# Kernel optimization log

Measured on AMD Instinct MI355X. Metric: run time of the kernel, lower is better.

The kernel has to match this reference:

```python
import jax, jax.numpy as jnp
import numpy as np

N = 100000
NNZ = 3200000
K = 3

def setup_inputs() -> dict:
    key = jax.random.key(0)
    ks = jax.random.split(key, 9)
    return {
        "x": jax.random.normal(ks[0], (N, 128), dtype=jnp.float32),
        "vals": jax.random.uniform(ks[1], (NNZ,), dtype=jnp.float32) * (1.0 / 32.0),
        "W1": jax.random.normal(ks[2], (128 * K, 256), dtype=jnp.float32) * 0.05,
        "b1": jax.random.normal(ks[3], (256,), dtype=jnp.float32) * 0.05,
        "W2": jax.random.normal(ks[4], (256 * K, 64), dtype=jnp.float32) * 0.05,
        "b2": jax.random.normal(ks[5], (64,), dtype=jnp.float32) * 0.05,
        "rows": jax.random.randint(ks[6], (NNZ,), 0, N, dtype=jnp.int32),
        "cols": jax.random.randint(ks[7], (NNZ,), 0, N, dtype=jnp.int32),
        "idx": jax.random.randint(ks[8], (50000,), 0, N, dtype=jnp.int32),
    }

def _spmm(rows, cols, vals, x):
    # sparse [N,N] @ dense [N,F] via gather + segment_sum
    return jax.ops.segment_sum(vals[:, None] * x[cols], rows, num_segments=N)

def _cheb_basis(x, rows, cols, vals, k):
    # Chebyshev recurrence: T0=x, T1=L x, T_m = 2 L T_{m-1} - T_{m-2}
    xs = [x]
    if k > 1:
        x0, x1 = x, _spmm(rows, cols, vals, x)
        xs.append(x1)
        for _ in range(2, k):
            x2 = 2.0 * _spmm(rows, cols, vals, x1) - x0
            xs.append(x2)
            x0, x1 = x1, x2
    # match torch layout: [N, F, K] -> [N, F*K] (per-feature K contiguous)
    return jnp.stack(xs, axis=2).reshape(x.shape[0], -1)

def reference(x, vals, W1, b1, W2, b2, rows, cols, idx):
    h = _cheb_basis(x, rows, cols, vals, K) @ W1 + b1
    h = jax.nn.relu(h)  # dropout omitted (eval mode)
    out = _cheb_basis(h, rows, cols, vals, K) @ W2 + b2
    return out[idx]
```

## Files before the change

kernel.cpp:

```cpp
#include <hip/hip_runtime.h>
#include <hip/hip_bf16.h>

typedef __attribute__((ext_vector_type(8))) __bf16 bf16x8;
typedef __attribute__((ext_vector_type(4))) float floatx4;
typedef unsigned short ushort_t;
typedef unsigned int uint_t;

#define N_NODES 100000
#define NNZ_E   3200000
#define N_IDX   50000
#define NB_BKT  196
#define PTILE   8192
#define PBLOCKS 391

__device__ __forceinline__ float bf2f(uint_t u16) {
  union { float f; uint_t i; } v; v.i = u16 << 16; return v.f;
}
__device__ __forceinline__ unsigned short f2bf(float f) {
  union { float f; uint_t i; } v; v.f = f;
  uint_t x = v.i;
  return (unsigned short)((x + 0x7FFFu + ((x >> 16) & 1u)) >> 16);
}
__device__ __forceinline__ uint_t pk(float lo, float hi) {
  return ((uint_t)f2bf(hi) << 16) | (uint_t)f2bf(lo);
}


__global__ __launch_bounds__(256) void k_bhist(const int* __restrict__ rows,
                                               int* __restrict__ bcnt) {
  __shared__ int h[NB_BKT];
  for (int i = threadIdx.x; i < NB_BKT; i += 256) h[i] = 0;
  __syncthreads();
  int base = blockIdx.x * PTILE;
  for (int i = threadIdx.x; i < PTILE; i += 256) {
    int e = base + i;
    if (e < NNZ_E) atomicAdd(&h[rows[e] >> 9], 1);
  }
  __syncthreads();
  for (int i = threadIdx.x; i < NB_BKT; i += 256)
    if (h[i]) atomicAdd(&bcnt[i], h[i]);
}

__global__ void k_bscan(const int* __restrict__ bcnt, int* __restrict__ bbase,
                        int* __restrict__ bcur) {
  __shared__ int ts[256];
  int t = threadIdx.x;
  int v = (t < NB_BKT) ? bcnt[t] : 0;
  ts[t] = v;
  __syncthreads();
  for (int off = 1; off < 256; off <<= 1) {
    int x = ts[t];
    int a = (t >= off) ? ts[t - off] : 0;
    __syncthreads();
    ts[t] = x + a;
    __syncthreads();
  }
  if (t < NB_BKT) {
    int b = (t == 0) ? 0 : ts[t - 1];
    bbase[t] = b;
    bcur[t] = b;
  }
}

__global__ __launch_bounds__(256) void k_part(const int* __restrict__ rows,
                                              const int* __restrict__ cols,
                                              const float* __restrict__ vals,
                                              int* __restrict__ bcur,
                                              int2* __restrict__ tmp) {
  __shared__ int h[NB_BKT];
  for (int i = threadIdx.x; i < NB_BKT; i += 256) h[i] = 0;
  __syncthreads();
  int base = blockIdx.x * PTILE;
  for (int i = threadIdx.x; i < PTILE; i += 256) {
    int e = base + i;
    if (e < NNZ_E) atomicAdd(&h[rows[e] >> 9], 1);
  }
  __syncthreads();
  for (int i = threadIdx.x; i < NB_BKT; i += 256) {
    int c = h[i];
    h[i] = c ? atomicAdd(&bcur[i], c) : 0;
  }
  __syncthreads();
  for (int i = threadIdx.x; i < PTILE; i += 256) {
    int e = base + i;
    if (e < NNZ_E) {
      int rr = rows[e];
      int p = atomicAdd(&h[rr >> 9], 1);
      int2 o;
      o.x = cols[e] | ((rr & 511) << 17);
      o.y = __float_as_int(vals[e]);
      tmp[p] = o;
    }
  }
}

__global__ __launch_bounds__(512) void k_sort(const int* __restrict__ bbase,
                                              const int2* __restrict__ tmp,
                                              int2* __restrict__ edges,
                                              int* __restrict__ rowptr) {
  __shared__ int cnt[512];
  __shared__ int ts[512];
  int b = blockIdx.x, t = threadIdx.x;
  int s = bbase[b];
  int epos = (b == NB_BKT - 1) ? NNZ_E : bbase[b + 1];
  cnt[t] = 0;
  __syncthreads();
  for (int i = s + t; i < epos; i += 512)
    atomicAdd(&cnt[(tmp[i].x >> 17) & 511], 1);
  __syncthreads();
  ts[t] = cnt[t];
  __syncthreads();
  for (int off = 1; off < 512; off <<= 1) {
    int x = ts[t];
    int a = (t >= off) ? ts[t - off] : 0;
    __syncthreads();
    ts[t] = x + a;
    __syncthreads();
  }
  int pre = (t == 0) ? 0 : ts[t - 1];
  int grow = b * 512 + t;
  if (grow < N_NODES) rowptr[grow] = s + pre;
  cnt[t] = s + pre;
  __syncthreads();
  for (int i = s + t; i < epos; i += 512) {
    int2 p = tmp[i];
    int rl = (p.x >> 17) & 511;
    int pos = atomicAdd(&cnt[rl], 1);
    int2 o;
    o.x = p.x & 0x1FFFF;
    o.y = p.y;
    edges[pos] = o;
  }
  if (b == 0 && t == 0) rowptr[N_NODES] = NNZ_E;
}


__global__ __launch_bounds__(256) void k_prep(
    const float4* __restrict__ x, const float* __restrict__ W1,
    const float* __restrict__ W2, ushort4* __restrict__ xb,
    ushort_t* __restrict__ W1p, ushort_t* __restrict__ W2p) {
  int b = blockIdx.x;
  if (b < 12500) {
    int i = b * 256 + threadIdx.x;
    float4 v = x[i];
    ushort4 o;
    o.x = f2bf(v.x); o.y = f2bf(v.y); o.z = f2bf(v.z); o.w = f2bf(v.w);
    xb[i] = o;
  } else if (b < 12884) {
    int kp = b - 12500;
    int n  = threadIdx.x;
    int ch = kp >> 7;
    int f  = kp & 127;
    float v;
    if (ch == 0)      v = W1[(f*3+0)*256+n] - W1[(f*3+2)*256+n];
    else if (ch == 1) v = W1[(f*3+1)*256+n];
    else              v = 2.0f * W1[(f*3+2)*256+n];
    int kb = kp >> 5, kr = kp & 31;
    int lane = ((kr >> 3) << 4) | (n & 15);
    W1p[(((size_t)kb * 16 + (n >> 4)) * 64 + lane) * 8 + (kr & 7)] = f2bf(v);
  } else {
    int f = b - 12884;
    int c = threadIdx.x;
    if (c < 192) {
      int g = c >> 6, n = c & 63;
      float v;
      if (g == 0)      v = W2[(f*3+0)*64+n] - W2[(f*3+2)*64+n];
      else if (g == 1) v = W2[(f*3+1)*64+n];
      else             v = 2.0f * W2[(f*3+2)*64+n];
      int kb = f >> 5, kr = f & 31;
      int nb = c >> 4;
      int lane = ((kr >> 3) << 4) | (c & 15);
      W2p[(((size_t)kb * 12 + nb) * 64 + lane) * 8 + (kr & 7)] = f2bf(v);
    }
  }
}


__global__ __launch_bounds__(256) void k_spmm128(
    const int* __restrict__ rowptr, const int2* __restrict__ edges,
    const ushort_t* __restrict__ in, ushort_t* __restrict__ out) {
  int r = __builtin_amdgcn_readfirstlane(blockIdx.x * 4 + (threadIdx.x >> 6));
  int f = threadIdx.x & 63;
  int e0 = rowptr[r], e1 = rowptr[r + 1];
  float a0 = 0.f, a1 = 0.f;
  int e = e0;
  for (; e + 16 <= e1; e += 16) {
    int2 E[16];
#pragma unroll
    for (int j = 0; j < 16; ++j) E[j] = edges[e + j];
    uint_t q[16];
#pragma unroll
    for (int j = 0; j < 16; ++j)
      q[j] = *(const uint_t*)(in + (size_t)E[j].x * 128 + 2 * f);
#pragma unroll
    for (int j = 0; j < 16; ++j) {
      float v = __int_as_float(E[j].y);
      a0 = fmaf(v, bf2f(q[j] & 0xFFFFu), a0);
      a1 = fmaf(v, bf2f(q[j] >> 16), a1);
    }
  }
  for (; e + 4 <= e1; e += 4) {
    int2 E[4];
#pragma unroll
    for (int j = 0; j < 4; ++j) E[j] = edges[e + j];
    uint_t q[4];
#pragma unroll
    for (int j = 0; j < 4; ++j)
      q[j] = *(const uint_t*)(in + (size_t)E[j].x * 128 + 2 * f);
#pragma unroll
    for (int j = 0; j < 4; ++j) {
      float v = __int_as_float(E[j].y);
      a0 = fmaf(v, bf2f(q[j] & 0xFFFFu), a0);
      a1 = fmaf(v, bf2f(q[j] >> 16), a1);
    }
  }
  for (; e < e1; ++e) {
    int2 E = edges[e];
    uint_t q = *(const uint_t*)(in + (size_t)E.x * 128 + 2 * f);
    float v = __int_as_float(E.y);
    a0 = fmaf(v, bf2f(q & 0xFFFFu), a0);
    a1 = fmaf(v, bf2f(q >> 16), a1);
  }
  uint_t o = ((uint_t)f2bf(a1) << 16) | (uint_t)f2bf(a0);
  *(uint_t*)(out + (size_t)r * 128 + 2 * f) = o;
}


__global__ __launch_bounds__(256) void k_spmm64_add(
    const int* __restrict__ rowptr, const int2* __restrict__ edges,
    const ushort_t* __restrict__ p2, const ushort_t* __restrict__ p1,
    ushort_t* __restrict__ u) {
  int r = __builtin_amdgcn_readfirstlane(blockIdx.x * 4 + (threadIdx.x >> 6));
  int lane = threadIdx.x & 63;
  int half = lane >> 5, l5 = lane & 31;
  int e0 = rowptr[r], e1 = rowptr[r + 1];
  float a0 = 0.f, a1 = 0.f;
  int e = e0;
  for (; e + 16 <= e1; e += 16) {
    int2 Ea[8], Eb[8];
#pragma unroll
    for (int j = 0; j < 8; ++j) { Ea[j] = edges[e + 2*j]; Eb[j] = edges[e + 2*j + 1]; }
    uint_t q[8];
#pragma unroll
    for (int j = 0; j < 8; ++j) {
      int c = half ? Eb[j].x : Ea[j].x;
      q[j] = *(const uint_t*)(p2 + (size_t)c * 64 + 2 * l5);
    }
#pragma unroll
    for (int j = 0; j < 8; ++j) {
      float v = __int_as_float(half ? Eb[j].y : Ea[j].y);
      a0 = fmaf(v, bf2f(q[j] & 0xFFFFu), a0);
      a1 = fmaf(v, bf2f(q[j] >> 16), a1);
    }
  }
  for (; e + 2 <= e1; e += 2) {
    int2 Ea = edges[e], Eb = edges[e + 1];
    int c = half ? Eb.x : Ea.x;
    uint_t q = *(const uint_t*)(p2 + (size_t)c * 64 + 2 * l5);
    float v = __int_as_float(half ? Eb.y : Ea.y);
    a0 = fmaf(v, bf2f(q & 0xFFFFu), a0);
    a1 = fmaf(v, bf2f(q >> 16), a1);
  }
  if (e < e1) {
    int2 Ea = edges[e];
    uint_t q = *(const uint_t*)(p2 + (size_t)Ea.x * 64 + 2 * l5);
    float v = half ? 0.f : __int_as_float(Ea.y);
    a0 = fmaf(v, bf2f(q & 0xFFFFu), a0);
    a1 = fmaf(v, bf2f(q >> 16), a1);
  }
  a0 += __shfl_xor(a0, 32);
  a1 += __shfl_xor(a1, 32);
  if (half == 0) {
    uint_t pp = *(const uint_t*)(p1 + (size_t)r * 64 + 2 * l5);
    float b0 = a0 + bf2f(pp & 0xFFFFu);
    float b1 = a1 + bf2f(pp >> 16);
    *(uint_t*)(u + (size_t)r * 64 + 2 * l5) = pk(b0, b1);
  }
}


__global__ __launch_bounds__(256) void k_spmm64_idx(
    const int* __restrict__ rowptr, const int2* __restrict__ edges,
    const ushort_t* __restrict__ u, const float* __restrict__ p0,
    const int* __restrict__ idx, float* __restrict__ out) {
  int o = __builtin_amdgcn_readfirstlane(blockIdx.x * 4 + (threadIdx.x >> 6));
  int lane = threadIdx.x & 63;
  int half = lane >> 5, l5 = lane & 31;
  int r = __builtin_amdgcn_readfirstlane(idx[o]);
  int e0 = rowptr[r], e1 = rowptr[r + 1];
  float a0 = 0.f, a1 = 0.f;
  int e = e0;
  for (; e + 16 <= e1; e += 16) {
    int2 Ea[8], Eb[8];
#pragma unroll
    for (int j = 0; j < 8; ++j) { Ea[j] = edges[e + 2*j]; Eb[j] = edges[e + 2*j + 1]; }
    uint_t q[8];
#pragma unroll
    for (int j = 0; j < 8; ++j) {
      int c = half ? Eb[j].x : Ea[j].x;
      q[j] = *(const uint_t*)(u + (size_t)c * 64 + 2 * l5);
    }
#pragma unroll
    for (int j = 0; j < 8; ++j) {
      float v = __int_as_float(half ? Eb[j].y : Ea[j].y);
      a0 = fmaf(v, bf2f(q[j] & 0xFFFFu), a0);
      a1 = fmaf(v, bf2f(q[j] >> 16), a1);
    }
  }
  for (; e + 2 <= e1; e += 2) {
    int2 Ea = edges[e], Eb = edges[e + 1];
    int c = half ? Eb.x : Ea.x;
    uint_t q = *(const uint_t*)(u + (size_t)c * 64 + 2 * l5);
    float v = __int_as_float(half ? Eb.y : Ea.y);
    a0 = fmaf(v, bf2f(q & 0xFFFFu), a0);
    a1 = fmaf(v, bf2f(q >> 16), a1);
  }
  if (e < e1) {
    int2 Ea = edges[e];
    uint_t q = *(const uint_t*)(u + (size_t)Ea.x * 64 + 2 * l5);
    float v = half ? 0.f : __int_as_float(Ea.y);
    a0 = fmaf(v, bf2f(q & 0xFFFFu), a0);
    a1 = fmaf(v, bf2f(q >> 16), a1);
  }
  a0 += __shfl_xor(a0, 32);
  a1 += __shfl_xor(a1, 32);
  if (half == 0) {
    float2 b = *(const float2*)(p0 + (size_t)r * 64 + 2 * l5);
    float2 ww; ww.x = b.x + a0; ww.y = b.y + a1;
    *(float2*)(out + (size_t)o * 64 + 2 * l5) = ww;
  }
}


__global__ __launch_bounds__(256) void k_gemm1(
    const ushort_t* __restrict__ A0, const ushort_t* __restrict__ A1,
    const ushort_t* __restrict__ A2, const ushort_t* __restrict__ Bp,
    const float* __restrict__ bias, ushort_t* __restrict__ h) {
  int lane = threadIdx.x & 63;
  int ng = threadIdx.x >> 6;
  int r0 = blockIdx.x * 64;
  int mrl = lane & 15;
  int ko = (lane >> 4) << 3;
  floatx4 acc[4][4] = {};
#pragma unroll
  for (int kbg = 0; kbg < 12; ++kbg) {
    int c = kbg >> 2, kb = kbg & 3;
    const ushort_t* Asrc = (c == 0 ? A0 : c == 1 ? A1 : A2);
    bf16x8 a[4];
#pragma unroll
    for (int mi = 0; mi < 4; ++mi) {
      int mr = r0 + mi * 16 + mrl;
      if (mr > N_NODES - 1) mr = N_NODES - 1;
      a[mi] = *(const bf16x8*)(Asrc + (size_t)mr * 128 + kb * 32 + ko);
    }
    const ushort_t* Bb = Bp + (((size_t)(kbg * 16 + ng * 4)) * 64 + lane) * 8;
#pragma unroll
    for (int nt = 0; nt < 4; ++nt) {
      bf16x8 b = *(const bf16x8*)(Bb + (size_t)nt * 64 * 8);
#pragma unroll
      for (int mi = 0; mi < 4; ++mi)
        acc[mi][nt] = __builtin_amdgcn_mfma_f32_16x16x32_bf16(a[mi], b, acc[mi][nt], 0, 0, 0);
    }
  }
  int col0 = ng * 64 + (lane & 15);
  int rr0 = (lane >> 4) << 2;
#pragma unroll
  for (int nt = 0; nt < 4; ++nt) {
    int col = col0 + nt * 16;
    float bv = bias[col];
#pragma unroll
    for (int mi = 0; mi < 4; ++mi) {
      int rb = r0 + mi * 16 + rr0;
#pragma unroll
      for (int rg = 0; rg < 4; ++rg) {
        int row = rb + rg;
        if (row < N_NODES) {
          float v = acc[mi][nt][rg] + bv;
          v = v > 0.f ? v : 0.f;
          h[(size_t)row * 256 + col] = f2bf(v);
        }
      }
    }
  }
}


__global__ __launch_bounds__(256) void k_gemm2(
    const ushort_t* __restrict__ A, const ushort_t* __restrict__ Bp,
    const float* __restrict__ bias, float* __restrict__ p0,
    ushort_t* __restrict__ p1, ushort_t* __restrict__ p2) {
  int wid = (blockIdx.x * 256 + threadIdx.x) >> 6;
  int lane = threadIdx.x & 63;
  int mt4 = wid / 3, ng = wid - mt4 * 3;
  if (mt4 >= 1563) return;
  int r0 = mt4 * 64;
  int mrl = lane & 15;
  int ko = (lane >> 4) << 3;
  floatx4 acc[4][4] = {};
#pragma unroll
  for (int kb = 0; kb < 8; ++kb) {
    bf16x8 a[4];
#pragma unroll
    for (int mi = 0; mi < 4; ++mi) {
      int mr = r0 + mi * 16 + mrl;
      if (mr > N_NODES - 1) mr = N_NODES - 1;
      a[mi] = *(const bf16x8*)(A + (size_t)mr * 256 + kb * 32 + ko);
    }
    const ushort_t* Bb = Bp + (((size_t)(kb * 12 + ng * 4)) * 64 + lane) * 8;
#pragma unroll
    for (int nt = 0; nt < 4; ++nt) {
      bf16x8 b = *(const bf16x8*)(Bb + (size_t)nt * 64 * 8);
#pragma unroll
      for (int mi = 0; mi < 4; ++mi)
        acc[mi][nt] = __builtin_amdgcn_mfma_f32_16x16x32_bf16(a[mi], b, acc[mi][nt], 0, 0, 0);
    }
  }
  int c16 = lane & 15;
  int rr0 = (lane >> 4) << 2;
  if (ng == 0) {
#pragma unroll
    for (int nt = 0; nt < 4; ++nt) {
      float bv = bias[nt * 16 + c16];
#pragma unroll
      for (int mi = 0; mi < 4; ++mi) {
        int rb = r0 + mi * 16 + rr0;
#pragma unroll
        for (int rg = 0; rg < 4; ++rg) {
          int row = rb + rg;
          if (row < N_NODES)
            p0[(size_t)row * 64 + nt * 16 + c16] = acc[mi][nt][rg] + bv;
        }
      }
    }
  } else {
    ushort_t* dst = (ng == 1) ? p1 : p2;
#pragma unroll
    for (int nt = 0; nt < 4; ++nt)
#pragma unroll
      for (int mi = 0; mi < 4; ++mi) {
        int rb = r0 + mi * 16 + rr0;
#pragma unroll
        for (int rg = 0; rg < 4; ++rg) {
          int row = rb + rg;
          if (row < N_NODES)
            dst[(size_t)row * 64 + nt * 16 + c16] = f2bf(acc[mi][nt][rg]);
        }
      }
  }
}


extern "C" void kernel_launch(void* const* d_in, const int* in_sizes, int n_in,
                              void* d_out, int out_size, void* d_ws, size_t ws_size,
                              hipStream_t stream) {
  const float* x    = (const float*)d_in[0];
  const float* vals = (const float*)d_in[1];
  const float* W1   = (const float*)d_in[2];
  const float* b1   = (const float*)d_in[3];
  const float* W2   = (const float*)d_in[4];
  const float* b2   = (const float*)d_in[5];
  const int*   rows = (const int*)d_in[6];
  const int*   cols = (const int*)d_in[7];
  const int*   idx  = (const int*)d_in[8];
  float* out = (float*)d_out;

  char* w = (char*)d_ws;
  size_t off = 0;
  auto take = [&](size_t b) -> char* {
    char* p = w + off;
    off += (b + 255) & ~(size_t)255;
    return p;
  };
  int*      bcnt    = (int*)take((size_t)NB_BKT * 4);
  int*      bbase   = (int*)take((size_t)NB_BKT * 4);
  int*      bcur    = (int*)take((size_t)NB_BKT * 4);
  int*      rowptr  = (int*)take((size_t)(N_NODES + 1) * 4);
  int2*     tmp     = (int2*)take((size_t)NNZ_E * 8);
  int2*     edges   = (int2*)take((size_t)NNZ_E * 8);
  ushort_t* xb      = (ushort_t*)take((size_t)N_NODES * 128 * 2);
  ushort_t* T1a     = (ushort_t*)take((size_t)N_NODES * 128 * 2);
  ushort_t* U1      = (ushort_t*)take((size_t)N_NODES * 128 * 2);
  ushort_t* h       = (ushort_t*)take((size_t)N_NODES * 256 * 2);
  ushort_t* W1p     = (ushort_t*)take((size_t)384 * 256 * 2);
  ushort_t* W2p     = (ushort_t*)take((size_t)256 * 192 * 2);

  float*    p0 = (float*)xb;
  ushort_t* p1 = T1a;
  ushort_t* p2 = T1a + (size_t)N_NODES * 64;
  ushort_t* u  = U1;

  hipMemsetAsync(bcnt, 0, (size_t)NB_BKT * 4, stream);
  k_bhist<<<PBLOCKS, 256, 0, stream>>>(rows, bcnt);
  k_bscan<<<1, 256, 0, stream>>>(bcnt, bbase, bcur);
  k_part<<<PBLOCKS, 256, 0, stream>>>(rows, cols, vals, bcur, tmp);
  k_sort<<<NB_BKT, 512, 0, stream>>>(bbase, tmp, edges, rowptr);

  k_prep<<<13140, 256, 0, stream>>>((const float4*)x, W1, W2, (ushort4*)xb, W1p, W2p);

  k_spmm128<<<N_NODES / 4, 256, 0, stream>>>(rowptr, edges, xb, T1a);
  k_spmm128<<<N_NODES / 4, 256, 0, stream>>>(rowptr, edges, T1a, U1);
  k_gemm1<<<1563, 256, 0, stream>>>(xb, T1a, U1, W1p, b1, h);

  k_gemm2<<<1173, 256, 0, stream>>>(h, W2p, b2, p0, p1, p2);
  k_spmm64_add<<<N_NODES / 4, 256, 0, stream>>>(rowptr, edges, p2, p1, u);
  k_spmm64_idx<<<N_IDX / 4, 256, 0, stream>>>(rowptr, edges, u, p0, idx, out);
}
```

Measured before the change: 675.3 us.

## Split 128-wide SpMM into feature halves with dual-edge lanes per wavefront

New measurement: 680.5 us. About the same (+0.8%).

```diff
diff --git a/kernel.cpp b/kernel.cpp
--- a/kernel.cpp
+++ b/kernel.cpp
@@ -176,53 +176,56 @@
 }
 
 
-__global__ __launch_bounds__(256) void k_spmm128(
+__global__ __launch_bounds__(256) void k_spmm128h(
     const int* __restrict__ rowptr, const int2* __restrict__ edges,
     const ushort_t* __restrict__ in, ushort_t* __restrict__ out) {
-  int r = __builtin_amdgcn_readfirstlane(blockIdx.x * 4 + (threadIdx.x >> 6));
-  int f = threadIdx.x & 63;
+  int bid = blockIdx.x;
+  int hf = (bid >= 25000) ? 1 : 0;
+  int rb = bid - hf * 25000;
+  int w = threadIdx.x >> 6;
+  int r = __builtin_amdgcn_readfirstlane(rb * 4 + w);
+  int lane = threadIdx.x & 63;
+  int half = lane >> 5, l5 = lane & 31;
   int e0 = rowptr[r], e1 = rowptr[r + 1];
+  const ushort_t* tab = in + hf * 64 + 2 * l5;
   float a0 = 0.f, a1 = 0.f;
   int e = e0;
   for (; e + 16 <= e1; e += 16) {
-    int2 E[16];
-#pragma unroll
-    for (int j = 0; j < 16; ++j) E[j] = edges[e + j];
-    uint_t q[16];
-#pragma unroll
-    for (int j = 0; j < 16; ++j)
-      q[j] = *(const uint_t*)(in + (size_t)E[j].x * 128 + 2 * f);
-#pragma unroll
-    for (int j = 0; j < 16; ++j) {
-      float v = __int_as_float(E[j].y);
+    int2 Ea[8], Eb[8];
+#pragma unroll
+    for (int j = 0; j < 8; ++j) { Ea[j] = edges[e + 2*j]; Eb[j] = edges[e + 2*j + 1]; }
+    uint_t q[8];
+#pragma unroll
+    for (int j = 0; j < 8; ++j) {
+      int c = half ? Eb[j].x : Ea[j].x;
+      q[j] = *(const uint_t*)(tab + (size_t)c * 128);
+    }
+#pragma unroll
+    for (int j = 0; j < 8; ++j) {
+      float v = __int_as_float(half ? Eb[j].y : Ea[j].y);
       a0 = fmaf(v, bf2f(q[j] & 0xFFFFu), a0);
       a1 = fmaf(v, bf2f(q[j] >> 16), a1);
     }
   }
-  for (; e + 4 <= e1; e += 4) {
-    int2 E[4];
-#pragma unroll
-    for (int j = 0; j < 4; ++j) E[j] = edges[e + j];
-    uint_t q[4];
-#pragma unroll
-    for (int j = 0; j < 4; ++j)
-      q[j] = *(const uint_t*)(in + (size_t)E[j].x * 128 + 2 * f);
-#pragma unroll
-    for (int j = 0; j < 4; ++j) {
-      float v = __int_as_float(E[j].y);
-      a0 = fmaf(v, bf2f(q[j] & 0xFFFFu), a0);
-      a1 = fmaf(v, bf2f(q[j] >> 16), a1);
-    }
-  }
-  for (; e < e1; ++e) {
-    int2 E = edges[e];
-    uint_t q = *(const uint_t*)(in + (size_t)E.x * 128 + 2 * f);
-    float v = __int_as_float(E.y);
+  for (; e + 2 <= e1; e += 2) {
+    int2 Ea = edges[e], Eb = edges[e + 1];
+    int c = half ? Eb.x : Ea.x;
+    uint_t q = *(const uint_t*)(tab + (size_t)c * 128);
+    float v = __int_as_float(half ? Eb.y : Ea.y);
     a0 = fmaf(v, bf2f(q & 0xFFFFu), a0);
     a1 = fmaf(v, bf2f(q >> 16), a1);
   }
-  uint_t o = ((uint_t)f2bf(a1) << 16) | (uint_t)f2bf(a0);
-  *(uint_t*)(out + (size_t)r * 128 + 2 * f) = o;
+  if (e < e1) {
+    int2 Ea = edges[e];
+    uint_t q = *(const uint_t*)(tab + (size_t)Ea.x * 128);
+    float v = half ? 0.f : __int_as_float(Ea.y);
+    a0 = fmaf(v, bf2f(q & 0xFFFFu), a0);
+    a1 = fmaf(v, bf2f(q >> 16), a1);
+  }
+  a0 += __shfl_xor(a0, 32);
+  a1 += __shfl_xor(a1, 32);
+  if (half == 0)
+    *(uint_t*)(out + (size_t)r * 128 + hf * 64 + 2 * l5) = pk(a0, a1);
 }
 
 
@@ -497,8 +500,8 @@
 
   k_prep<<<13140, 256, 0, stream>>>((const float4*)x, W1, W2, (ushort4*)xb, W1p, W2p);
 
-  k_spmm128<<<N_NODES / 4, 256, 0, stream>>>(rowptr, edges, xb, T1a);
-  k_spmm128<<<N_NODES / 4, 256, 0, stream>>>(rowptr, edges, T1a, U1);
+  k_spmm128h<<<N_NODES / 4 * 2, 256, 0, stream>>>(rowptr, edges, xb, T1a);
+  k_spmm128h<<<N_NODES / 4 * 2, 256, 0, stream>>>(rowptr, edges, T1a, U1);
   k_gemm1<<<1563, 256, 0, stream>>>(xb, T1a, U1, W1p, b1, h);
 
   k_gemm2<<<1173, 256, 0, stream>>>(h, W2p, b2, p0, p1, p2);
```
